# Performance work log

Hardware: AMD Instinct MI355X
Metric: run time of the kernel (lower is better)

The kernel has to match this reference:

```python
import jax, jax.numpy as jnp
import numpy as np


def setup_inputs() -> dict:
    key = jax.random.key(0)
    ks = jax.random.split(key, 5)
    B, S, E2, D = 64, 1024, 1024, 512  # E2 = 2*enc_hid_dim
    hidden = jax.random.normal(ks[0], (B, D), dtype=jnp.float32)
    encoder_outputs = jax.random.normal(ks[1], (B, S, E2), dtype=jnp.float32)
    mask = jnp.ones((B, S), dtype=jnp.int32)
    attn_W = jax.random.normal(ks[2], (E2 + D, D), dtype=jnp.float32) * 0.02
    attn_b = jax.random.normal(ks[3], (D,), dtype=jnp.float32) * 0.02
    v_W = jax.random.normal(ks[4], (D,), dtype=jnp.float32) * 0.02
    return {"hidden": hidden, "encoder_outputs": encoder_outputs, "mask": mask,
            "attn_W": attn_W, "attn_b": attn_b, "v_W": v_W}


def reference(hidden, encoder_outputs, mask, attn_W, attn_b, v_W):
    # cat((hidden_repeated, enc_out)) @ attn_W  ==  hidden @ W_h + enc_out @ W_e
    D = hidden.shape[-1]
    W_h = attn_W[-D:]          # [D, D]   (decoder-hidden part of concat)
    W_e = attn_W[:-D]          # [2E, D]  (encoder-output part)
    # Note: torch concat order is (hidden, encoder_outputs), so split accordingly.
    W_hid = attn_W[: D] if False else attn_W[:D]
    # concat order: hidden first -> rows [0:D] are hidden's, rows [D:] are encoder's
    W_h = attn_W[:D]           # [D, D]
    W_e = attn_W[D:]           # [2E, D]
    h_proj = hidden @ W_h                                   # [B, D]
    e_proj = jnp.einsum('bse,ed->bsd', encoder_outputs, W_e)  # [B, S, D]
    energy = jnp.tanh(e_proj + h_proj[:, None, :] + attn_b)   # [B, S, D]
    scores = jnp.einsum('bsd,d->bs', energy, v_W)             # [B, S]
    neg_inf = jnp.finfo(scores.dtype).min
    scores = jnp.where(mask == 0, neg_inf, scores)
    attn_weights = jax.nn.softmax(scores, axis=1)             # [B, S]
    context = jnp.einsum('bs,bse->be', attn_weights, encoder_outputs)  # [B, 2E]
    return context, attn_weights
```

## Files before the change

kernel.cpp:

```cpp
#include <hip/hip_runtime.h>
#include <hip/hip_bf16.h>


typedef __attribute__((ext_vector_type(4))) float f32x4;
typedef __attribute__((ext_vector_type(8))) short short8;
typedef __attribute__((ext_vector_type(8))) __bf16 bf16x8;

__device__ __forceinline__ void gload_lds16(const void* g, void* l) {
  __builtin_amdgcn_global_load_lds(
      (const __attribute__((address_space(1))) unsigned int*)g,
      (__attribute__((address_space(3))) unsigned int*)l,
      16, 0, 0);
}

__device__ __forceinline__ unsigned short f2bf_rne(float f) {
  union { float f; unsigned int u; } v; v.f = f;
  unsigned int r = v.u + 0x7FFFu + ((v.u >> 16) & 1u);
  return (unsigned short)(r >> 16);
}

__device__ __forceinline__ float fast_tanh(float x) {
  float e = __expf(2.0f * x);
  return 1.0f - 2.0f * __builtin_amdgcn_rcpf(e + 1.0f);
}

__global__ void hproj_kernel(const float* __restrict__ hidden,
                             const float* __restrict__ attn_W,
                             float* __restrict__ hb ) {
  int b = blockIdx.x >> 2, kc = blockIdx.x & 3;
  int tid = threadIdx.x;
  __shared__ float hrow[128];
  if (tid < 128) hrow[tid] = hidden[b * 512 + kc * 128 + tid];
  __syncthreads();
  const float* Wp = attn_W + (size_t)(kc * 128) * 512;
  float a0 = 0.f, a1 = 0.f;
#pragma unroll 4
  for (int k = 0; k < 128; ++k) {
    float h = hrow[k];
    a0 = fmaf(h, Wp[(size_t)k * 512 + tid], a0);
    a1 = fmaf(h, Wp[(size_t)k * 512 + tid + 256], a1);
  }
  atomicAdd(&hb[b * 512 + tid], a0);
  atomicAdd(&hb[b * 512 + tid + 256], a1);
}

__global__ void wet_kernel(const float* __restrict__ attn_W,
                           unsigned short* __restrict__ weT) {
  __shared__ float tile[64][65];
  int bx = blockIdx.x;
  int kt = bx & 15;
  int nt = bx >> 4;
  int tid = threadIdx.x;
  int j = tid & 63, i = tid >> 6;
  const float* src = attn_W + (size_t)(512 + kt * 64) * 512 + nt * 64;
#pragma unroll
  for (int p = 0; p < 16; ++p) {
    int r = p * 4 + i;
    tile[r][j] = src[(size_t)r * 512 + j];
  }
  __syncthreads();
  unsigned short* dst = weT + (size_t)(nt * 64) * 1024 + kt * 64;
#pragma unroll
  for (int p = 0; p < 16; ++p) {
    int c = p * 4 + i;
    dst[(size_t)c * 1024 + j] = f2bf_rne(tile[j][c]);
  }
}

__global__ __launch_bounds__(256, 4) void fused_score_gemm(
    const float* __restrict__ enc,
    const unsigned short* __restrict__ weT,
    const float* __restrict__ hb,
    const float* __restrict__ attn_b,
    const float* __restrict__ vW,
    float* __restrict__ scores)
{
  __shared__ unsigned short At[128 * 64];
  __shared__ unsigned short Bt[128 * 64];

  int bx = blockIdx.x;
  int wg = ((bx & 7) << 8) | (bx >> 3);
  int m0 = (wg >> 2) << 7;
  int n0 = (wg & 3) << 7;

  int tid = threadIdx.x;
  int w = tid >> 6, l = tid & 63;
  int g = l >> 4, l15 = l & 15;
  int wm = (w >> 1) << 6, wn = (w & 1) << 6;

  int arow = tid >> 3;
  int aps = tid & 7;
  int asg = aps ^ (arow & 7);
  int aoff0 = arow * 1024 + asg * 8;

  int brow = ((w << 6) | l) >> 3;
  int bps = l & 7;
  int bsg = bps ^ ((l >> 3) & 7);
  int boff0 = brow * 1024 + bsg * 8;

  const float* Ab = enc + (size_t)m0 * 1024;
  const unsigned short* Bb = weT + (size_t)n0 * 1024;

  f32x4 zero = {0.f, 0.f, 0.f, 0.f};
  f32x4 acc[4][4];
#pragma unroll
  for (int i = 0; i < 4; ++i)
#pragma unroll
    for (int j = 0; j < 4; ++j) acc[i][j] = zero;

  int aRd[4], bRd[4];
#pragma unroll
  for (int mt = 0; mt < 4; ++mt) {
    int row = wm + mt * 16 + l15;
    aRd[mt] = row * 128 + ((g ^ (row & 7)) << 4);
  }
#pragma unroll
  for (int nt = 0; nt < 4; ++nt) {
    int row = wn + nt * 16 + l15;
    bRd[nt] = row * 128 + ((g ^ (row & 7)) << 4);
  }

  const char* Atc = (const char*)At;
  const char* Btc = (const char*)Bt;

  f32x4 rA[8];
#pragma unroll
  for (int i = 0; i < 4; ++i) {
    rA[2 * i]     = *(const f32x4*)(Ab + aoff0 + i * 32768);
    rA[2 * i + 1] = *(const f32x4*)(Ab + aoff0 + i * 32768 + 4);
  }

  for (int kt = 0; kt < 16; ++kt) {
    int k0n = (kt + (kt < 15)) << 6;
    __syncthreads();
#pragma unroll
    for (int i = 0; i < 4; ++i) {
      bf16x8 v;
      v[0] = (__bf16)rA[2 * i][0]; v[1] = (__bf16)rA[2 * i][1];
      v[2] = (__bf16)rA[2 * i][2]; v[3] = (__bf16)rA[2 * i][3];
      v[4] = (__bf16)rA[2 * i + 1][0]; v[5] = (__bf16)rA[2 * i + 1][1];
      v[6] = (__bf16)rA[2 * i + 1][2]; v[7] = (__bf16)rA[2 * i + 1][3];
      *(short8*)((char*)At + (i << 12) + (tid << 4)) = __builtin_bit_cast(short8, v);
    }
#pragma unroll
    for (int i = 0; i < 4; ++i)
      gload_lds16(Bb + boff0 + i * 32768 + (kt << 6),
                  (char*)Bt + ((i * 4 + w) << 10));
    __syncthreads();
#pragma unroll
    for (int i = 0; i < 4; ++i) {
      rA[2 * i]     = *(const f32x4*)(Ab + aoff0 + i * 32768 + k0n);
      rA[2 * i + 1] = *(const f32x4*)(Ab + aoff0 + i * 32768 + k0n + 4);
    }
#pragma unroll
    for (int kk = 0; kk < 2; ++kk) {
      int kx = kk << 6;
      short8 af[4], bfm[4];
#pragma unroll
      for (int mt = 0; mt < 4; ++mt)
        af[mt] = *(const short8*)(Atc + (aRd[mt] ^ kx));
#pragma unroll
      for (int nt = 0; nt < 4; ++nt)
        bfm[nt] = *(const short8*)(Btc + (bRd[nt] ^ kx));
#pragma unroll
      for (int mt = 0; mt < 4; ++mt)
#pragma unroll
        for (int nt = 0; nt < 4; ++nt)
          acc[mt][nt] = __builtin_amdgcn_mfma_f32_16x16x32_bf16(
              af[mt], bfm[nt], acc[mt][nt], 0, 0, 0);
    }
  }

  int b = m0 >> 10;
  float hbv[4], vwv[4];
#pragma unroll
  for (int nt = 0; nt < 4; ++nt) {
    int d = n0 + wn + nt * 16 + l15;
    hbv[nt] = hb[(b << 9) + d] + attn_b[d];
    vwv[nt] = vW[d];
  }
#pragma unroll
  for (int mt = 0; mt < 4; ++mt) {
#pragma unroll
    for (int j = 0; j < 4; ++j) {
      float p = 0.f;
#pragma unroll
      for (int nt = 0; nt < 4; ++nt)
        p = fmaf(fast_tanh(acc[mt][nt][j] + hbv[nt]), vwv[nt], p);
      p += __shfl_xor(p, 1);
      p += __shfl_xor(p, 2);
      p += __shfl_xor(p, 4);
      p += __shfl_xor(p, 8);
      if (l15 == 0)
        atomicAdd(&scores[m0 + wm + mt * 16 + (g << 2) + j], p);
    }
  }
}

__global__ void softmax_kernel(const float* __restrict__ scores,
                               const int* __restrict__ mask,
                               float* __restrict__ attn_out) {
  int b = blockIdx.x, tid = threadIdx.x;
  __shared__ float red[256];
  const float NEG = -3.402823466e38f;
  float v[4];
  float mx = NEG;
#pragma unroll
  for (int i = 0; i < 4; ++i) {
    int s = (i << 8) + tid;
    float sc = scores[(b << 10) + s];
    v[i] = (mask[(b << 10) + s] == 0) ? NEG : sc;
    mx = fmaxf(mx, v[i]);
  }
  red[tid] = mx; __syncthreads();
  for (int off = 128; off > 0; off >>= 1) {
    if (tid < off) red[tid] = fmaxf(red[tid], red[tid + off]);
    __syncthreads();
  }
  mx = red[0]; __syncthreads();
  float sum = 0.f;
#pragma unroll
  for (int i = 0; i < 4; ++i) { v[i] = __expf(v[i] - mx); sum += v[i]; }
  red[tid] = sum; __syncthreads();
  for (int off = 128; off > 0; off >>= 1) {
    if (tid < off) red[tid] += red[tid + off];
    __syncthreads();
  }
  float inv = 1.f / red[0];
#pragma unroll
  for (int i = 0; i < 4; ++i)
    attn_out[(b << 10) + (i << 8) + tid] = v[i] * inv;
}

__global__ void context_kernel(const float* __restrict__ wts,
                               const float* __restrict__ enc,
                               float* __restrict__ ctx ) {
  int bx = blockIdx.x;
  int b = bx >> 4, sch = bx & 15;
  int tid = threadIdx.x;
  const float* encp = enc + ((size_t)(b << 10) + (sch << 6)) * 1024 + (tid << 2);
  const float* wp = wts + (b << 10) + (sch << 6);
  f32x4 a0 = {0.f, 0.f, 0.f, 0.f}, a1 = a0, a2 = a0, a3 = a0;
  for (int s = 0; s < 64; s += 4) {
    float w0 = wp[s], w1 = wp[s + 1], w2 = wp[s + 2], w3 = wp[s + 3];
    f32x4 v0 = *(const f32x4*)(encp + ((size_t)(s + 0) << 10));
    f32x4 v1 = *(const f32x4*)(encp + ((size_t)(s + 1) << 10));
    f32x4 v2 = *(const f32x4*)(encp + ((size_t)(s + 2) << 10));
    f32x4 v3 = *(const f32x4*)(encp + ((size_t)(s + 3) << 10));
#pragma unroll
    for (int j = 0; j < 4; ++j) {
      a0[j] = fmaf(w0, v0[j], a0[j]);
      a1[j] = fmaf(w1, v1[j], a1[j]);
      a2[j] = fmaf(w2, v2[j], a2[j]);
      a3[j] = fmaf(w3, v3[j], a3[j]);
    }
  }
  float* dst = ctx + (b << 10) + (tid << 2);
#pragma unroll
  for (int j = 0; j < 4; ++j)
    atomicAdd(&dst[j], a0[j] + a1[j] + a2[j] + a3[j]);
}

extern "C" void kernel_launch(void* const* d_in, const int* in_sizes, int n_in,
                              void* d_out, int out_size, void* d_ws, size_t ws_size,
                              hipStream_t stream) {
  const float* hidden = (const float*)d_in[0];
  const float* enc    = (const float*)d_in[1];
  const int*   mask   = (const int*)d_in[2];
  const float* attn_W = (const float*)d_in[3];
  const float* attn_b = (const float*)d_in[4];
  const float* vW     = (const float*)d_in[5];
  float* out = (float*)d_out;

  float* scores = (float*)d_ws;
  float* hb     = scores + 65536;
  unsigned short* weT = (unsigned short*)(hb + 32768);

  hipMemsetAsync(d_ws, 0, (65536 + 32768) * sizeof(float), stream);
  hipMemsetAsync(d_out, 0, 65536 * sizeof(float), stream);

  hproj_kernel<<<256, 256, 0, stream>>>(hidden, attn_W, hb);
  wet_kernel<<<128, 256, 0, stream>>>(attn_W, weT);
  fused_score_gemm<<<2048, 256, 0, stream>>>(enc, weT, hb, attn_b, vW, scores);
  softmax_kernel<<<64, 256, 0, stream>>>(scores, mask, out + 65536);
  context_kernel<<<1024, 256, 0, stream>>>(out + 65536, enc, out);
}
```

Measured before the change: 485.3 us.

## Fuse score GEMM, per-strip softmax and context into one kernel with combine

Each workgroup now computes the full 512-wide N dimension for a 128-row strip, so the tanh/v reduction completes in LDS instead of through global atomics. The kernel then computes a local max/sum softmax over the strip and immediately forms a partial context from the encoder rows it just loaded, which should still be cache-resident. A small combine kernel merges the partial maxima, sums and contexts flash-style and writes the weights. This removes the separate softmax and context passes, a second full read of the encoder outputs, and the memsets and atomics. In exchange it uses larger workgroups with more LDS and registers (acc[4][8], a 64 KB B tile), which lowers occupancy.

```diff
diff --git a/kernel.cpp b/kernel.cpp
--- a/kernel.cpp
+++ b/kernel.cpp
@@ -3,6 +3,7 @@
 
 
 typedef __attribute__((ext_vector_type(4))) float f32x4;
+typedef __attribute__((ext_vector_type(2))) float f32x2;
 typedef __attribute__((ext_vector_type(8))) short short8;
 typedef __attribute__((ext_vector_type(8))) __bf16 bf16x8;
 
@@ -67,115 +68,120 @@
   }
 }
 
-__global__ __launch_bounds__(256, 4) void fused_score_gemm(
+__global__ __launch_bounds__(512, 2) void fused_score_ctx(
     const float* __restrict__ enc,
     const unsigned short* __restrict__ weT,
     const float* __restrict__ hb,
     const float* __restrict__ attn_b,
     const float* __restrict__ vW,
-    float* __restrict__ scores)
+    const int* __restrict__ mask,
+    float* __restrict__ scores,
+    float* __restrict__ pmax,
+    float* __restrict__ psum,
+    float* __restrict__ pctx)
 {
   __shared__ unsigned short At[128 * 64];
-  __shared__ unsigned short Bt[128 * 64];
-
+  __shared__ unsigned short Bt[512 * 64];
+  __shared__ float sc[4][128];
+  __shared__ float parr[128];
+  __shared__ float redm[2], reds[2];
+
+  const float NEG = -3.402823466e38f;
   int bx = blockIdx.x;
-  int wg = ((bx & 7) << 8) | (bx >> 3);
-  int m0 = (wg >> 2) << 7;
-  int n0 = (wg & 3) << 7;
+  int strip = ((bx & 7) << 6) | (bx >> 3);
+  int m0 = strip << 7;
+  int b = m0 >> 10;
 
   int tid = threadIdx.x;
   int w = tid >> 6, l = tid & 63;
   int g = l >> 4, l15 = l & 15;
-  int wm = (w >> 1) << 6, wn = (w & 1) << 6;
-
-  int arow = tid >> 3;
-  int aps = tid & 7;
-  int asg = aps ^ (arow & 7);
-  int aoff0 = arow * 1024 + asg * 8;
-
-  int brow = ((w << 6) | l) >> 3;
-  int bps = l & 7;
-  int bsg = bps ^ ((l >> 3) & 7);
-  int boff0 = brow * 1024 + bsg * 8;
-
-  const float* Ab = enc + (size_t)m0 * 1024;
-  const unsigned short* Bb = weT + (size_t)n0 * 1024;
+  int wm = w >> 2, wn = w & 3;
+
+  int arow = tid >> 2;
+  int as0 = (tid & 3) << 1;
+  const float* Ap = enc + (size_t)(m0 + arow) * 1024 + (as0 << 3);
+  int awb0 = arow * 128 + ((as0 ^ (arow & 7)) << 4);
+  int awb1 = arow * 128 + (((as0 + 1) ^ (arow & 7)) << 4);
+
+  int brow0 = tid >> 3;
+  int bs = (tid & 7) ^ (brow0 & 7);
+  const unsigned short* Bp = weT + (size_t)brow0 * 1024 + (bs << 3);
 
   f32x4 zero = {0.f, 0.f, 0.f, 0.f};
-  f32x4 acc[4][4];
+  f32x4 acc[4][8];
 #pragma unroll
   for (int i = 0; i < 4; ++i)
 #pragma unroll
-    for (int j = 0; j < 4; ++j) acc[i][j] = zero;
-
-  int aRd[4], bRd[4];
+    for (int j = 0; j < 8; ++j) acc[i][j] = zero;
+
+  int aRd[4], bRd[8];
 #pragma unroll
   for (int mt = 0; mt < 4; ++mt) {
-    int row = wm + mt * 16 + l15;
+    int row = wm * 64 + mt * 16 + l15;
     aRd[mt] = row * 128 + ((g ^ (row & 7)) << 4);
   }
 #pragma unroll
-  for (int nt = 0; nt < 4; ++nt) {
-    int row = wn + nt * 16 + l15;
+  for (int nt = 0; nt < 8; ++nt) {
+    int row = wn * 128 + nt * 16 + l15;
     bRd[nt] = row * 128 + ((g ^ (row & 7)) << 4);
   }
 
   const char* Atc = (const char*)At;
   const char* Btc = (const char*)Bt;
 
-  f32x4 rA[8];
-#pragma unroll
-  for (int i = 0; i < 4; ++i) {
-    rA[2 * i]     = *(const f32x4*)(Ab + aoff0 + i * 32768);
-    rA[2 * i + 1] = *(const f32x4*)(Ab + aoff0 + i * 32768 + 4);
-  }
+  f32x4 rA0 = *(const f32x4*)(Ap + 0);
+  f32x4 rA1 = *(const f32x4*)(Ap + 4);
+  f32x4 rA2 = *(const f32x4*)(Ap + 8);
+  f32x4 rA3 = *(const f32x4*)(Ap + 12);
 
   for (int kt = 0; kt < 16; ++kt) {
     int k0n = (kt + (kt < 15)) << 6;
     __syncthreads();
-#pragma unroll
-    for (int i = 0; i < 4; ++i) {
-      bf16x8 v;
-      v[0] = (__bf16)rA[2 * i][0]; v[1] = (__bf16)rA[2 * i][1];
-      v[2] = (__bf16)rA[2 * i][2]; v[3] = (__bf16)rA[2 * i][3];
-      v[4] = (__bf16)rA[2 * i + 1][0]; v[5] = (__bf16)rA[2 * i + 1][1];
-      v[6] = (__bf16)rA[2 * i + 1][2]; v[7] = (__bf16)rA[2 * i + 1][3];
-      *(short8*)((char*)At + (i << 12) + (tid << 4)) = __builtin_bit_cast(short8, v);
+    {
+      bf16x8 v0, v1;
+      v0[0] = (__bf16)rA0[0]; v0[1] = (__bf16)rA0[1];
+      v0[2] = (__bf16)rA0[2]; v0[3] = (__bf16)rA0[3];
+      v0[4] = (__bf16)rA1[0]; v0[5] = (__bf16)rA1[1];
+      v0[6] = (__bf16)rA1[2]; v0[7] = (__bf16)rA1[3];
+      v1[0] = (__bf16)rA2[0]; v1[1] = (__bf16)rA2[1];
+      v1[2] = (__bf16)rA2[2]; v1[3] = (__bf16)rA2[3];
+      v1[4] = (__bf16)rA3[0]; v1[5] = (__bf16)rA3[1];
+      v1[6] = (__bf16)rA3[2]; v1[7] = (__bf16)rA3[3];
+      *(short8*)((char*)At + awb0) = __builtin_bit_cast(short8, v0);
+      *(short8*)((char*)At + awb1) = __builtin_bit_cast(short8, v1);
     }
 #pragma unroll
-    for (int i = 0; i < 4; ++i)
-      gload_lds16(Bb + boff0 + i * 32768 + (kt << 6),
-                  (char*)Bt + ((i * 4 + w) << 10));
+    for (int i = 0; i < 8; ++i)
+      gload_lds16(Bp + (i << 16) + (kt << 6),
+                  (char*)Bt + (i << 13) + (w << 10));
     __syncthreads();
-#pragma unroll
-    for (int i = 0; i < 4; ++i) {
-      rA[2 * i]     = *(const f32x4*)(Ab + aoff0 + i * 32768 + k0n);
-      rA[2 * i + 1] = *(const f32x4*)(Ab + aoff0 + i * 32768 + k0n + 4);
-    }
+    rA0 = *(const f32x4*)(Ap + k0n + 0);
+    rA1 = *(const f32x4*)(Ap + k0n + 4);
+    rA2 = *(const f32x4*)(Ap + k0n + 8);
+    rA3 = *(const f32x4*)(Ap + k0n + 12);
 #pragma unroll
     for (int kk = 0; kk < 2; ++kk) {
       int kx = kk << 6;
-      short8 af[4], bfm[4];
+      short8 af[4], bfm[8];
 #pragma unroll
       for (int mt = 0; mt < 4; ++mt)
         af[mt] = *(const short8*)(Atc + (aRd[mt] ^ kx));
 #pragma unroll
-      for (int nt = 0; nt < 4; ++nt)
+      for (int nt = 0; nt < 8; ++nt)
         bfm[nt] = *(const short8*)(Btc + (bRd[nt] ^ kx));
 #pragma unroll
       for (int mt = 0; mt < 4; ++mt)
 #pragma unroll
-        for (int nt = 0; nt < 4; ++nt)
+        for (int nt = 0; nt < 8; ++nt)
           acc[mt][nt] = __builtin_amdgcn_mfma_f32_16x16x32_bf16(
               af[mt], bfm[nt], acc[mt][nt], 0, 0, 0);
     }
   }
 
-  int b = m0 >> 10;
-  float hbv[4], vwv[4];
-#pragma unroll
-  for (int nt = 0; nt < 4; ++nt) {
-    int d = n0 + wn + nt * 16 + l15;
+  float hbv[8], vwv[8];
+#pragma unroll
+  for (int nt = 0; nt < 8; ++nt) {
+    int d = wn * 128 + nt * 16 + l15;
     hbv[nt] = hb[(b << 9) + d] + attn_b[d];
     vwv[nt] = vW[d];
   }
@@ -185,80 +191,91 @@
     for (int j = 0; j < 4; ++j) {
       float p = 0.f;
 #pragma unroll
-      for (int nt = 0; nt < 4; ++nt)
+      for (int nt = 0; nt < 8; ++nt)
         p = fmaf(fast_tanh(acc[mt][nt][j] + hbv[nt]), vwv[nt], p);
       p += __shfl_xor(p, 1);
       p += __shfl_xor(p, 2);
       p += __shfl_xor(p, 4);
       p += __shfl_xor(p, 8);
       if (l15 == 0)
-        atomicAdd(&scores[m0 + wm + mt * 16 + (g << 2) + j], p);
+        sc[wn][wm * 64 + mt * 16 + (g << 2) + j] = p;
     }
   }
-}
-
-__global__ void softmax_kernel(const float* __restrict__ scores,
-                               const int* __restrict__ mask,
-                               float* __restrict__ attn_out) {
+  __syncthreads();
+
+  float s4 = 0.f;
+  if (tid < 128) {
+    s4 = sc[0][tid] + sc[1][tid] + sc[2][tid] + sc[3][tid];
+    int gm = m0 + tid;
+    if (mask[gm] == 0) s4 = NEG;
+    scores[gm] = s4;
+    float mx = s4;
+#pragma unroll
+    for (int off = 1; off < 64; off <<= 1) mx = fmaxf(mx, __shfl_xor(mx, off));
+    if (l == 0) redm[w] = mx;
+  }
+  __syncthreads();
+  if (tid < 128) {
+    float M_i = fmaxf(redm[0], redm[1]);
+    float pex = __expf(s4 - M_i);
+    parr[tid] = pex;
+    float sm = pex;
+#pragma unroll
+    for (int off = 1; off < 64; off <<= 1) sm += __shfl_xor(sm, off);
+    if (l == 0) reds[w] = sm;
+  }
+  __syncthreads();
+  if (tid == 0) {
+    pmax[strip] = fmaxf(redm[0], redm[1]);
+    psum[strip] = reds[0] + reds[1];
+  }
+
+  float c0 = 0.f, c1 = 0.f;
+  const float* ep = enc + (size_t)m0 * 1024 + (tid << 1);
+#pragma unroll 4
+  for (int s = 0; s < 128; ++s) {
+    float ps = parr[s];
+    f32x2 v = *(const f32x2*)(ep + ((size_t)s << 10));
+    c0 = fmaf(ps, v[0], c0);
+    c1 = fmaf(ps, v[1], c1);
+  }
+  float* pc = pctx + ((size_t)strip << 10) + (tid << 1);
+  pc[0] = c0; pc[1] = c1;
+}
+
+__global__ void combine_kernel(const float* __restrict__ scores,
+                               const float* __restrict__ pmax,
+                               const float* __restrict__ psum,
+                               const float* __restrict__ pctx,
+                               float* __restrict__ out) {
   int b = blockIdx.x, tid = threadIdx.x;
-  __shared__ float red[256];
-  const float NEG = -3.402823466e38f;
-  float v[4];
-  float mx = NEG;
-#pragma unroll
-  for (int i = 0; i < 4; ++i) {
-    int s = (i << 8) + tid;
-    float sc = scores[(b << 10) + s];
-    v[i] = (mask[(b << 10) + s] == 0) ? NEG : sc;
-    mx = fmaxf(mx, v[i]);
-  }
-  red[tid] = mx; __syncthreads();
-  for (int off = 128; off > 0; off >>= 1) {
-    if (tid < off) red[tid] = fmaxf(red[tid], red[tid + off]);
-    __syncthreads();
-  }
-  mx = red[0]; __syncthreads();
-  float sum = 0.f;
-#pragma unroll
-  for (int i = 0; i < 4; ++i) { v[i] = __expf(v[i] - mx); sum += v[i]; }
-  red[tid] = sum; __syncthreads();
-  for (int off = 128; off > 0; off >>= 1) {
-    if (tid < off) red[tid] += red[tid + off];
-    __syncthreads();
-  }
-  float inv = 1.f / red[0];
-#pragma unroll
-  for (int i = 0; i < 4; ++i)
-    attn_out[(b << 10) + (i << 8) + tid] = v[i] * inv;
-}
-
-__global__ void context_kernel(const float* __restrict__ wts,
-                               const float* __restrict__ enc,
-                               float* __restrict__ ctx ) {
-  int bx = blockIdx.x;
-  int b = bx >> 4, sch = bx & 15;
-  int tid = threadIdx.x;
-  const float* encp = enc + ((size_t)(b << 10) + (sch << 6)) * 1024 + (tid << 2);
-  const float* wp = wts + (b << 10) + (sch << 6);
-  f32x4 a0 = {0.f, 0.f, 0.f, 0.f}, a1 = a0, a2 = a0, a3 = a0;
-  for (int s = 0; s < 64; s += 4) {
-    float w0 = wp[s], w1 = wp[s + 1], w2 = wp[s + 2], w3 = wp[s + 3];
-    f32x4 v0 = *(const f32x4*)(encp + ((size_t)(s + 0) << 10));
-    f32x4 v1 = *(const f32x4*)(encp + ((size_t)(s + 1) << 10));
-    f32x4 v2 = *(const f32x4*)(encp + ((size_t)(s + 2) << 10));
-    f32x4 v3 = *(const f32x4*)(encp + ((size_t)(s + 3) << 10));
-#pragma unroll
-    for (int j = 0; j < 4; ++j) {
-      a0[j] = fmaf(w0, v0[j], a0[j]);
-      a1[j] = fmaf(w1, v1[j], a1[j]);
-      a2[j] = fmaf(w2, v2[j], a2[j]);
-      a3[j] = fmaf(w3, v3[j], a3[j]);
-    }
-  }
-  float* dst = ctx + (b << 10) + (tid << 2);
-#pragma unroll
-  for (int j = 0; j < 4; ++j)
-    atomicAdd(&dst[j], a0[j] + a1[j] + a2[j] + a3[j]);
+  float m8[8];
+  float M = pmax[b * 8];
+  m8[0] = M;
+#pragma unroll
+  for (int i = 1; i < 8; ++i) { m8[i] = pmax[b * 8 + i]; M = fmaxf(M, m8[i]); }
+  float e8[8]; float L = 0.f;
+#pragma unroll
+  for (int i = 0; i < 8; ++i) {
+    e8[i] = __expf(m8[i] - M);
+    L = fmaf(e8[i], psum[b * 8 + i], L);
+  }
+  float invL = 1.f / L;
+  f32x4 a = {0.f, 0.f, 0.f, 0.f};
+#pragma unroll
+  for (int i = 0; i < 8; ++i) {
+    f32x4 v = *(const f32x4*)(pctx + (size_t)(b * 8 + i) * 1024 + (tid << 2));
+#pragma unroll
+    for (int j = 0; j < 4; ++j) a[j] = fmaf(e8[i], v[j], a[j]);
+  }
+#pragma unroll
+  for (int j = 0; j < 4; ++j) a[j] *= invL;
+  *(f32x4*)(out + (b << 10) + (tid << 2)) = a;
+  f32x4 sv = *(const f32x4*)(scores + (b << 10) + (tid << 2));
+  f32x4 wv;
+#pragma unroll
+  for (int j = 0; j < 4; ++j) wv[j] = __expf(sv[j] - M) * invL;
+  *(f32x4*)(out + 65536 + (b << 10) + (tid << 2)) = wv;
 }
 
 extern "C" void kernel_launch(void* const* d_in, const int* in_sizes, int n_in,
@@ -275,13 +292,15 @@
   float* scores = (float*)d_ws;
   float* hb     = scores + 65536;
   unsigned short* weT = (unsigned short*)(hb + 32768);
-
-  hipMemsetAsync(d_ws, 0, (65536 + 32768) * sizeof(float), stream);
-  hipMemsetAsync(d_out, 0, 65536 * sizeof(float), stream);
+  float* pmax = (float*)(weT + 524288);
+  float* psum = pmax + 512;
+  float* pctx = psum + 512;
+
+  hipMemsetAsync(hb, 0, 32768 * sizeof(float), stream);
 
   hproj_kernel<<<256, 256, 0, stream>>>(hidden, attn_W, hb);
   wet_kernel<<<128, 256, 0, stream>>>(attn_W, weT);
-  fused_score_gemm<<<2048, 256, 0, stream>>>(enc, weT, hb, attn_b, vW, scores);
-  softmax_kernel<<<64, 256, 0, stream>>>(scores, mask, out + 65536);
-  context_kernel<<<1024, 256, 0, stream>>>(out + 65536, enc, out);
-}
+  fused_score_ctx<<<512, 512, 0, stream>>>(enc, weT, hb, attn_b, vW, mask,
+                                           scores, pmax, psum, pctx);
+  combine_kernel<<<64, 256, 0, stream>>>(scores, pmax, psum, pctx, out);
+}
```

New measurement: 487.0 us. Within noise of the previous version (+0.4%).
